# Kernel tuning notes

Hardware: AMD Instinct MI355X
Metric: run time of the kernel (lower is better)

Reference implementation:

```python
import jax, jax.numpy as jnp
import numpy as np

EPS = 1e-5

def setup_inputs() -> dict:
    key = jax.random.key(0)
    k1, k2 = jax.random.split(key)
    N, D, O = 32768, 4096, 256
    x = jax.random.normal(k1, (N, D), dtype=jnp.float32)
    gamma = jnp.ones((D,), dtype=jnp.float32)
    beta = jnp.zeros((D,), dtype=jnp.float32)
    W = jax.random.normal(k2, (O, D), dtype=jnp.float32) * (1.0 / np.sqrt(D))
    b = jnp.zeros((O,), dtype=jnp.float32)
    return {"x": x, "gamma": gamma, "beta": beta, "W": W, "b": b}


def reference(x, gamma, beta, W, b):
    # BatchNorm1d in training mode: per-feature batch mean and biased variance
    mean = jnp.mean(x, axis=0)                      # [D]
    var = jnp.mean(jnp.square(x - mean), axis=0)    # [D], biased (divide by N)
    xhat = (x - mean) * jax.lax.rsqrt(var + EPS)
    h = jax.nn.relu(xhat * gamma + beta)            # [N, D]
    # Linear projection
    return h @ W.T + b                               # [N, O]
```

## Files before the change

kernel.cpp:

```cpp
#include <hip/hip_runtime.h>
#include <hip/hip_bf16.h>

#define NROWS 32768
#define DDIM  4096
#define ODIM  256
#define EPSV  1e-5f

#define CHUNKS 128
#define RPC    256

#define BM 128
#define BK 64

typedef __attribute__((ext_vector_type(4))) float          f32x4;
typedef __attribute__((ext_vector_type(8))) __bf16         bf16x8;
typedef __attribute__((ext_vector_type(8))) unsigned short u16x8;
typedef __attribute__((ext_vector_type(4))) unsigned short u16x4;

static __device__ __forceinline__ unsigned short f2bf(float f) {
  return __builtin_bit_cast(unsigned short, __float2bfloat16(f));
}

__global__ __launch_bounds__(256) void k1_stats(const float* __restrict__ x,
                                                float* __restrict__ psum,
                                                float* __restrict__ psq) {
  const int col = blockIdx.x * 1024 + threadIdx.x * 4;
  const float* p = x + (size_t)blockIdx.y * RPC * DDIM + col;
  f32x4 s = {0.f, 0.f, 0.f, 0.f};
  f32x4 q = {0.f, 0.f, 0.f, 0.f};
#pragma unroll 8
  for (int r = 0; r < RPC; ++r) {
    f32x4 v = *(const f32x4*)p;
    p += DDIM;
    s += v;
    q += v * v;
  }
  *(f32x4*)(psum + (size_t)blockIdx.y * DDIM + col) = s;
  *(f32x4*)(psq  + (size_t)blockIdx.y * DDIM + col) = q;
}

__global__ __launch_bounds__(256) void k2_stats_finalize(
    const float* __restrict__ psum, const float* __restrict__ psq,
    const float* __restrict__ gamma, const float* __restrict__ beta,
    float* __restrict__ scale, float* __restrict__ shift) {
  __shared__ float ss[4][64];
  __shared__ float sq[4][64];
  const int lane = threadIdx.x & 63;
  const int g    = threadIdx.x >> 6;
  const int d    = blockIdx.x * 64 + lane;
  float s = 0.f, qq = 0.f;
  for (int c = g * 32; c < (g + 1) * 32; ++c) {
    s  += psum[(size_t)c * DDIM + d];
    qq += psq [(size_t)c * DDIM + d];
  }
  ss[g][lane] = s;
  sq[g][lane] = qq;
  __syncthreads();
  if (g == 0) {
    s  = ss[0][lane] + ss[1][lane] + ss[2][lane] + ss[3][lane];
    qq = sq[0][lane] + sq[1][lane] + sq[2][lane] + sq[3][lane];
    const float inv = 1.0f / (float)NROWS;
    const float mean = s * inv;
    const float var  = fmaxf(qq * inv - mean * mean, 0.f);
    const float a = gamma[d] * rsqrtf(var + EPSV);
    scale[d] = a;
    shift[d] = beta[d] - mean * a;
  }
}

__global__ __launch_bounds__(256) void k2_wconv(const float* __restrict__ Wf,
                                                unsigned short* __restrict__ Wb) {
  const size_t i = ((size_t)blockIdx.x * 256 + threadIdx.x) * 4;
  f32x4 v = *(const f32x4*)(Wf + i);
  u16x4 o;
  o[0] = f2bf(v[0]); o[1] = f2bf(v[1]); o[2] = f2bf(v[2]); o[3] = f2bf(v[3]);
  *(u16x4*)(Wb + i) = o;
}

__global__ __launch_bounds__(512, 2) void k3_bn_gemm(
    const float* __restrict__ x,
    const unsigned short* __restrict__ Wb,
    const float* __restrict__ scale,
    const float* __restrict__ shift,
    const float* __restrict__ bias,
    float* __restrict__ out) {
  __shared__ unsigned short As[BM * BK];
  __shared__ unsigned short Bs[ODIM * BK];

  const int tid = threadIdx.x;
  const int l   = tid & 63;
  const int w   = tid >> 6;
  const int wr  = w >> 2;
  const int wc  = w & 3;
  const size_t bm0 = (size_t)blockIdx.x * BM;

  const int rA = tid >> 3;
  const int uA = tid & 7;
  const float* xp0 = x + (bm0 + rA) * (size_t)DDIM + uA * 8;
  const float* xp1 = xp0 + (size_t)64 * DDIM;
  unsigned short* aw0 = &As[rA * 64 + ((uA ^ (rA & 7)) << 3)];
  unsigned short* aw1 = aw0 + 64 * 64;
  const float* sp = scale + uA * 8;
  const float* cp = shift + uA * 8;

  const unsigned short* bsrc[4];
  unsigned short* bdst[4];
#pragma unroll
  for (int q = 0; q < 4; ++q) {
    const int p  = w * 256 + q * 64 + l;
    const int o  = p >> 3;
    const int up = p & 7;
    bsrc[q] = Wb + (size_t)o * DDIM + ((up ^ (o & 7)) << 3);
    bdst[q] = &Bs[(w * 256 + q * 64) * 8];
  }

  int offA[4], offB[4];
#pragma unroll
  for (int i = 0; i < 4; ++i) {
    const int row = wr * 64 + i * 16 + (l & 15);
    offA[i] = row * 64 + (((l >> 4) ^ (row & 7)) << 3);
  }
#pragma unroll
  for (int j = 0; j < 4; ++j) {
    const int row = wc * 64 + j * 16 + (l & 15);
    offB[j] = row * 64 + (((l >> 4) ^ (row & 7)) << 3);
  }

  const f32x4 zero = {0.f, 0.f, 0.f, 0.f};
  f32x4 acc[4][4];
#pragma unroll
  for (int i = 0; i < 4; ++i)
#pragma unroll
    for (int j = 0; j < 4; ++j) acc[i][j] = zero;

  for (int kt = 0; kt < DDIM / BK; ++kt) {
#pragma unroll
    for (int q = 0; q < 4; ++q) {
      __builtin_amdgcn_global_load_lds(
          (__attribute__((address_space(1))) void*)bsrc[q],
          (__attribute__((address_space(3))) void*)bdst[q], 16, 0, 0);
      bsrc[q] += BK;
    }
    f32x4 sa0 = *(const f32x4*)sp;
    f32x4 sa1 = *(const f32x4*)(sp + 4);
    f32x4 sc0 = *(const f32x4*)cp;
    f32x4 sc1 = *(const f32x4*)(cp + 4);
    f32x4 v00 = *(const f32x4*)xp0;
    f32x4 v01 = *(const f32x4*)(xp0 + 4);
    f32x4 v10 = *(const f32x4*)xp1;
    f32x4 v11 = *(const f32x4*)(xp1 + 4);
    sp += BK; cp += BK; xp0 += BK; xp1 += BK;
    u16x8 pk0, pk1;
#pragma unroll
    for (int e = 0; e < 4; ++e) {
      pk0[e]     = f2bf(fmaxf(v00[e] * sa0[e] + sc0[e], 0.f));
      pk0[e + 4] = f2bf(fmaxf(v01[e] * sa1[e] + sc1[e], 0.f));
      pk1[e]     = f2bf(fmaxf(v10[e] * sa0[e] + sc0[e], 0.f));
      pk1[e + 4] = f2bf(fmaxf(v11[e] * sa1[e] + sc1[e], 0.f));
    }
    *(u16x8*)aw0 = pk0;
    *(u16x8*)aw1 = pk1;

    __syncthreads();

#pragma unroll
    for (int kk = 0; kk < 2; ++kk) {
      const int kx = kk << 5;
      bf16x8 af[4], bf[4];
#pragma unroll
      for (int i = 0; i < 4; ++i)
        af[i] = __builtin_bit_cast(bf16x8, *(const u16x8*)&As[offA[i] ^ kx]);
#pragma unroll
      for (int j = 0; j < 4; ++j)
        bf[j] = __builtin_bit_cast(bf16x8, *(const u16x8*)&Bs[offB[j] ^ kx]);
#pragma unroll
      for (int i = 0; i < 4; ++i)
#pragma unroll
        for (int j = 0; j < 4; ++j)
          acc[i][j] = __builtin_amdgcn_mfma_f32_16x16x32_bf16(af[i], bf[j], acc[i][j], 0, 0, 0);
    }

    __syncthreads();
  }

  const int cl = l & 15;
  const int rg = l >> 4;
#pragma unroll
  for (int j = 0; j < 4; ++j) {
    const int oc = wc * 64 + j * 16 + cl;
    const float bv = bias[oc];
#pragma unroll
    for (int i = 0; i < 4; ++i) {
      const size_t r0 = bm0 + wr * 64 + i * 16 + rg * 4;
#pragma unroll
      for (int rr = 0; rr < 4; ++rr) {
        out[(r0 + rr) * ODIM + oc] = acc[i][j][rr] + bv;
      }
    }
  }
}

extern "C" void kernel_launch(void* const* d_in, const int* in_sizes, int n_in,
                              void* d_out, int out_size, void* d_ws, size_t ws_size,
                              hipStream_t stream) {
  const float* x     = (const float*)d_in[0];
  const float* gamma = (const float*)d_in[1];
  const float* beta  = (const float*)d_in[2];
  const float* W     = (const float*)d_in[3];
  const float* b     = (const float*)d_in[4];
  float* out = (float*)d_out;

  float* psum  = (float*)d_ws;
  float* psq   = psum + (size_t)CHUNKS * DDIM;
  float* scale = psum + 2 * (size_t)CHUNKS * DDIM;
  float* shift = scale + DDIM;
  unsigned short* Wb = (unsigned short*)(shift + DDIM);

  k1_stats<<<dim3(4, CHUNKS), 256, 0, stream>>>(x, psum, psq);
  k2_stats_finalize<<<DDIM / 64, 256, 0, stream>>>(psum, psq, gamma, beta, scale, shift);
  k2_wconv<<<(ODIM * DDIM) / 1024, 256, 0, stream>>>(W, Wb);
  k3_bn_gemm<<<NROWS / BM, 512, 0, stream>>>(x, Wb, scale, shift, b, out);
}
```

Before: 260.9 us.

## Double-buffer GEMM LDS tiles with register prefetch and widen stats grid

The fused BN+GEMM kernel now uses two LDS buffers for the A and B tiles. It issues the next tile's global loads of x and W before running the MFMAs on the current tile, then writes the normalized bf16 values into the other buffer, so only one barrier per k-step is needed. The launch bound drops to one block per CU because LDS use doubles, which trades occupancy for software overlap of memory and compute. The stats kernel also switches to 2-wide loads and twice as many blocks to spread the column-sum pass across more workgroups.

After: 285.9 us. 1.1x slower.

```diff
diff --git a/kernel.cpp b/kernel.cpp
--- a/kernel.cpp
+++ b/kernel.cpp
@@ -11,7 +11,9 @@
 
 #define BM 128
 #define BK 64
-
+#define NKT (DDIM / BK)
+
+typedef __attribute__((ext_vector_type(2))) float          f32x2;
 typedef __attribute__((ext_vector_type(4))) float          f32x4;
 typedef __attribute__((ext_vector_type(8))) __bf16         bf16x8;
 typedef __attribute__((ext_vector_type(8))) unsigned short u16x8;
@@ -24,19 +26,19 @@
 __global__ __launch_bounds__(256) void k1_stats(const float* __restrict__ x,
                                                 float* __restrict__ psum,
                                                 float* __restrict__ psq) {
-  const int col = blockIdx.x * 1024 + threadIdx.x * 4;
+  const int col = blockIdx.x * 512 + threadIdx.x * 2;
   const float* p = x + (size_t)blockIdx.y * RPC * DDIM + col;
-  f32x4 s = {0.f, 0.f, 0.f, 0.f};
-  f32x4 q = {0.f, 0.f, 0.f, 0.f};
+  f32x2 s = {0.f, 0.f};
+  f32x2 q = {0.f, 0.f};
 #pragma unroll 8
   for (int r = 0; r < RPC; ++r) {
-    f32x4 v = *(const f32x4*)p;
+    f32x2 v = *(const f32x2*)p;
     p += DDIM;
     s += v;
     q += v * v;
   }
-  *(f32x4*)(psum + (size_t)blockIdx.y * DDIM + col) = s;
-  *(f32x4*)(psq  + (size_t)blockIdx.y * DDIM + col) = q;
+  *(f32x2*)(psum + (size_t)blockIdx.y * DDIM + col) = s;
+  *(f32x2*)(psq  + (size_t)blockIdx.y * DDIM + col) = q;
 }
 
 __global__ __launch_bounds__(256) void k2_stats_finalize(
@@ -77,15 +79,15 @@
   *(u16x4*)(Wb + i) = o;
 }
 
-__global__ __launch_bounds__(512, 2) void k3_bn_gemm(
+__global__ __launch_bounds__(512, 1) void k3_bn_gemm(
     const float* __restrict__ x,
     const unsigned short* __restrict__ Wb,
     const float* __restrict__ scale,
     const float* __restrict__ shift,
     const float* __restrict__ bias,
     float* __restrict__ out) {
-  __shared__ unsigned short As[BM * BK];
-  __shared__ unsigned short Bs[ODIM * BK];
+  __shared__ unsigned short As[2][BM * BK];
+  __shared__ unsigned short Bs[2][ODIM * BK];
 
   const int tid = threadIdx.x;
   const int l   = tid & 63;
@@ -98,20 +100,17 @@
   const int uA = tid & 7;
   const float* xp0 = x + (bm0 + rA) * (size_t)DDIM + uA * 8;
   const float* xp1 = xp0 + (size_t)64 * DDIM;
-  unsigned short* aw0 = &As[rA * 64 + ((uA ^ (rA & 7)) << 3)];
-  unsigned short* aw1 = aw0 + 64 * 64;
+  const int awo = rA * 64 + ((uA ^ (rA & 7)) << 3);
   const float* sp = scale + uA * 8;
   const float* cp = shift + uA * 8;
 
   const unsigned short* bsrc[4];
-  unsigned short* bdst[4];
 #pragma unroll
   for (int q = 0; q < 4; ++q) {
     const int p  = w * 256 + q * 64 + l;
     const int o  = p >> 3;
     const int up = p & 7;
     bsrc[q] = Wb + (size_t)o * DDIM + ((up ^ (o & 7)) << 3);
-    bdst[q] = &Bs[(w * 256 + q * 64) * 8];
   }
 
   int offA[4], offB[4];
@@ -133,23 +132,24 @@
 #pragma unroll
     for (int j = 0; j < 4; ++j) acc[i][j] = zero;
 
-  for (int kt = 0; kt < DDIM / BK; ++kt) {
-#pragma unroll
-    for (int q = 0; q < 4; ++q) {
-      __builtin_amdgcn_global_load_lds(
-          (__attribute__((address_space(1))) void*)bsrc[q],
-          (__attribute__((address_space(3))) void*)bdst[q], 16, 0, 0);
-      bsrc[q] += BK;
-    }
+  {
+    f32x4 v00 = *(const f32x4*)xp0;
+    f32x4 v01 = *(const f32x4*)(xp0 + 4);
+    f32x4 v10 = *(const f32x4*)xp1;
+    f32x4 v11 = *(const f32x4*)(xp1 + 4);
     f32x4 sa0 = *(const f32x4*)sp;
     f32x4 sa1 = *(const f32x4*)(sp + 4);
     f32x4 sc0 = *(const f32x4*)cp;
     f32x4 sc1 = *(const f32x4*)(cp + 4);
-    f32x4 v00 = *(const f32x4*)xp0;
-    f32x4 v01 = *(const f32x4*)(xp0 + 4);
-    f32x4 v10 = *(const f32x4*)xp1;
-    f32x4 v11 = *(const f32x4*)(xp1 + 4);
-    sp += BK; cp += BK; xp0 += BK; xp1 += BK;
+    xp0 += BK; xp1 += BK; sp += BK; cp += BK;
+#pragma unroll
+    for (int q = 0; q < 4; ++q) {
+      __builtin_amdgcn_global_load_lds(
+          (__attribute__((address_space(1))) void*)bsrc[q],
+          (__attribute__((address_space(3))) void*)(&Bs[0][(w * 256 + q * 64) * 8]),
+          16, 0, 0);
+      bsrc[q] += BK;
+    }
     u16x8 pk0, pk1;
 #pragma unroll
     for (int e = 0; e < 4; ++e) {
@@ -158,30 +158,75 @@
       pk1[e]     = f2bf(fmaxf(v10[e] * sa0[e] + sc0[e], 0.f));
       pk1[e + 4] = f2bf(fmaxf(v11[e] * sa1[e] + sc1[e], 0.f));
     }
-    *(u16x8*)aw0 = pk0;
-    *(u16x8*)aw1 = pk1;
-
+    *(u16x8*)&As[0][awo]        = pk0;
+    *(u16x8*)&As[0][awo + 4096] = pk1;
     __syncthreads();
-
-#pragma unroll
-    for (int kk = 0; kk < 2; ++kk) {
-      const int kx = kk << 5;
-      bf16x8 af[4], bf[4];
-#pragma unroll
-      for (int i = 0; i < 4; ++i)
-        af[i] = __builtin_bit_cast(bf16x8, *(const u16x8*)&As[offA[i] ^ kx]);
-#pragma unroll
-      for (int j = 0; j < 4; ++j)
-        bf[j] = __builtin_bit_cast(bf16x8, *(const u16x8*)&Bs[offB[j] ^ kx]);
-#pragma unroll
-      for (int i = 0; i < 4; ++i)
-#pragma unroll
-        for (int j = 0; j < 4; ++j)
-          acc[i][j] = __builtin_amdgcn_mfma_f32_16x16x32_bf16(af[i], bf[j], acc[i][j], 0, 0, 0);
-    }
-
-    __syncthreads();
-  }
+  }
+
+#define STEP(BUFI, PF)                                                         \
+  do {                                                                         \
+    f32x4 v00, v01, v10, v11, sa0, sa1, sc0, sc1;                              \
+    if (PF) {                                                                  \
+      v00 = *(const f32x4*)xp0;                                                \
+      v01 = *(const f32x4*)(xp0 + 4);                                          \
+      v10 = *(const f32x4*)xp1;                                                \
+      v11 = *(const f32x4*)(xp1 + 4);                                          \
+      sa0 = *(const f32x4*)sp;                                                 \
+      sa1 = *(const f32x4*)(sp + 4);                                           \
+      sc0 = *(const f32x4*)cp;                                                 \
+      sc1 = *(const f32x4*)(cp + 4);                                           \
+      xp0 += BK; xp1 += BK; sp += BK; cp += BK;                                \
+      _Pragma("unroll")                                                        \
+      for (int q = 0; q < 4; ++q) {                                            \
+        __builtin_amdgcn_global_load_lds(                                      \
+            (__attribute__((address_space(1))) void*)bsrc[q],                  \
+            (__attribute__((address_space(3))) void*)(                         \
+                &Bs[(BUFI) ^ 1][(w * 256 + q * 64) * 8]),                      \
+            16, 0, 0);                                                         \
+        bsrc[q] += BK;                                                         \
+      }                                                                        \
+    }                                                                          \
+    _Pragma("unroll")                                                          \
+    for (int kk = 0; kk < 2; ++kk) {                                           \
+      const int kx = kk << 5;                                                  \
+      bf16x8 af[4], bfr[4];                                                    \
+      _Pragma("unroll")                                                        \
+      for (int i = 0; i < 4; ++i)                                              \
+        af[i] = __builtin_bit_cast(bf16x8,                                     \
+                                   *(const u16x8*)&As[BUFI][offA[i] ^ kx]);    \
+      _Pragma("unroll")                                                        \
+      for (int j = 0; j < 4; ++j)                                              \
+        bfr[j] = __builtin_bit_cast(bf16x8,                                    \
+                                    *(const u16x8*)&Bs[BUFI][offB[j] ^ kx]);   \
+      _Pragma("unroll")                                                        \
+      for (int i = 0; i < 4; ++i)                                              \
+        _Pragma("unroll")                                                      \
+        for (int j = 0; j < 4; ++j)                                            \
+          acc[i][j] = __builtin_amdgcn_mfma_f32_16x16x32_bf16(                 \
+              af[i], bfr[j], acc[i][j], 0, 0, 0);                              \
+    }                                                                          \
+    if (PF) {                                                                  \
+      u16x8 pk0, pk1;                                                          \
+      _Pragma("unroll")                                                        \
+      for (int e = 0; e < 4; ++e) {                                            \
+        pk0[e]     = f2bf(fmaxf(v00[e] * sa0[e] + sc0[e], 0.f));               \
+        pk0[e + 4] = f2bf(fmaxf(v01[e] * sa1[e] + sc1[e], 0.f));               \
+        pk1[e]     = f2bf(fmaxf(v10[e] * sa0[e] + sc0[e], 0.f));               \
+        pk1[e + 4] = f2bf(fmaxf(v11[e] * sa1[e] + sc1[e], 0.f));               \
+      }                                                                        \
+      *(u16x8*)&As[(BUFI) ^ 1][awo]        = pk0;                              \
+      *(u16x8*)&As[(BUFI) ^ 1][awo + 4096] = pk1;                              \
+    }                                                                          \
+    __syncthreads();                                                           \
+  } while (0)
+
+  for (int kt = 0; kt < NKT - 2; kt += 2) {
+    STEP(0, true);
+    STEP(1, true);
+  }
+  STEP(0, true);
+  STEP(1, false);
+#undef STEP
 
   const int cl = l & 15;
   const int rg = l >> 4;
@@ -216,7 +261,7 @@
   float* shift = scale + DDIM;
   unsigned short* Wb = (unsigned short*)(shift + DDIM);
 
-  k1_stats<<<dim3(4, CHUNKS), 256, 0, stream>>>(x, psum, psq);
+  k1_stats<<<dim3(8, CHUNKS), 256, 0, stream>>>(x, psum, psq);
   k2_stats_finalize<<<DDIM / 64, 256, 0, stream>>>(psum, psq, gamma, beta, scale, shift);
   k2_wconv<<<(ODIM * DDIM) / 1024, 256, 0, stream>>>(W, Wb);
   k3_bn_gemm<<<NROWS / BM, 512, 0, stream>>>(x, Wb, scale, shift, b, out);
```

## Double-buffer LDS tiles and prefetch next K-tile during MFMA phase

Applied to the files above, without the earlier changes.

Restructures the fused BN+GEMM main loop into a two-stage software pipeline. The next tile's x loads (via inline-asm global loads) and W global-to-LDS copies are issued before the current tile's MFMAs, with explicit waitcnt and barriers so there is one barrier per step instead of two. Scale and shift are staged into shared memory once per block. The larger LDS footprint (double buffers plus 32 KB of scale/shift) forces occupancy down to one block per CU, and the handwritten waitcnt logic could be fragile.

Measured after the change: 239.2 us (median of 2 runs). 8.3% less time.

```diff
diff --git a/kernel.cpp b/kernel.cpp
--- a/kernel.cpp
+++ b/kernel.cpp
@@ -11,6 +11,7 @@
 
 #define BM 128
 #define BK 64
+#define NKT (DDIM / BK)
 
 typedef __attribute__((ext_vector_type(4))) float          f32x4;
 typedef __attribute__((ext_vector_type(8))) __bf16         bf16x8;
@@ -77,15 +78,17 @@
   *(u16x4*)(Wb + i) = o;
 }
 
-__global__ __launch_bounds__(512, 2) void k3_bn_gemm(
+__global__ __launch_bounds__(512, 1) void k3_bn_gemm(
     const float* __restrict__ x,
     const unsigned short* __restrict__ Wb,
     const float* __restrict__ scale,
     const float* __restrict__ shift,
     const float* __restrict__ bias,
     float* __restrict__ out) {
-  __shared__ unsigned short As[BM * BK];
-  __shared__ unsigned short Bs[ODIM * BK];
+  __shared__ unsigned short As[2][BM * BK];
+  __shared__ unsigned short Bs[2][ODIM * BK];
+  __shared__ float SF[DDIM];
+  __shared__ float SH[DDIM];
 
   const int tid = threadIdx.x;
   const int l   = tid & 63;
@@ -94,24 +97,25 @@
   const int wc  = w & 3;
   const size_t bm0 = (size_t)blockIdx.x * BM;
 
+  ((f32x4*)SF)[tid * 2]     = ((const f32x4*)scale)[tid * 2];
+  ((f32x4*)SF)[tid * 2 + 1] = ((const f32x4*)scale)[tid * 2 + 1];
+  ((f32x4*)SH)[tid * 2]     = ((const f32x4*)shift)[tid * 2];
+  ((f32x4*)SH)[tid * 2 + 1] = ((const f32x4*)shift)[tid * 2 + 1];
+
   const int rA = tid >> 3;
   const int uA = tid & 7;
   const float* xp0 = x + (bm0 + rA) * (size_t)DDIM + uA * 8;
   const float* xp1 = xp0 + (size_t)64 * DDIM;
-  unsigned short* aw0 = &As[rA * 64 + ((uA ^ (rA & 7)) << 3)];
-  unsigned short* aw1 = aw0 + 64 * 64;
-  const float* sp = scale + uA * 8;
-  const float* cp = shift + uA * 8;
+  const int awo = rA * 64 + ((uA ^ (rA & 7)) << 3);
+  int ktb = uA * 8;
 
   const unsigned short* bsrc[4];
-  unsigned short* bdst[4];
 #pragma unroll
   for (int q = 0; q < 4; ++q) {
     const int p  = w * 256 + q * 64 + l;
     const int o  = p >> 3;
     const int up = p & 7;
     bsrc[q] = Wb + (size_t)o * DDIM + ((up ^ (o & 7)) << 3);
-    bdst[q] = &Bs[(w * 256 + q * 64) * 8];
   }
 
   int offA[4], offB[4];
@@ -133,55 +137,110 @@
 #pragma unroll
     for (int j = 0; j < 4; ++j) acc[i][j] = zero;
 
-  for (int kt = 0; kt < DDIM / BK; ++kt) {
-#pragma unroll
-    for (int q = 0; q < 4; ++q) {
-      __builtin_amdgcn_global_load_lds(
-          (__attribute__((address_space(1))) void*)bsrc[q],
-          (__attribute__((address_space(3))) void*)bdst[q], 16, 0, 0);
-      bsrc[q] += BK;
-    }
-    f32x4 sa0 = *(const f32x4*)sp;
-    f32x4 sa1 = *(const f32x4*)(sp + 4);
-    f32x4 sc0 = *(const f32x4*)cp;
-    f32x4 sc1 = *(const f32x4*)(cp + 4);
-    f32x4 v00 = *(const f32x4*)xp0;
-    f32x4 v01 = *(const f32x4*)(xp0 + 4);
-    f32x4 v10 = *(const f32x4*)xp1;
-    f32x4 v11 = *(const f32x4*)(xp1 + 4);
-    sp += BK; cp += BK; xp0 += BK; xp1 += BK;
-    u16x8 pk0, pk1;
-#pragma unroll
-    for (int e = 0; e < 4; ++e) {
-      pk0[e]     = f2bf(fmaxf(v00[e] * sa0[e] + sc0[e], 0.f));
-      pk0[e + 4] = f2bf(fmaxf(v01[e] * sa1[e] + sc1[e], 0.f));
-      pk1[e]     = f2bf(fmaxf(v10[e] * sa0[e] + sc0[e], 0.f));
-      pk1[e + 4] = f2bf(fmaxf(v11[e] * sa1[e] + sc1[e], 0.f));
-    }
-    *(u16x8*)aw0 = pk0;
-    *(u16x8*)aw1 = pk1;
-
-    __syncthreads();
-
-#pragma unroll
-    for (int kk = 0; kk < 2; ++kk) {
-      const int kx = kk << 5;
-      bf16x8 af[4], bf[4];
-#pragma unroll
-      for (int i = 0; i < 4; ++i)
-        af[i] = __builtin_bit_cast(bf16x8, *(const u16x8*)&As[offA[i] ^ kx]);
-#pragma unroll
-      for (int j = 0; j < 4; ++j)
-        bf[j] = __builtin_bit_cast(bf16x8, *(const u16x8*)&Bs[offB[j] ^ kx]);
-#pragma unroll
-      for (int i = 0; i < 4; ++i)
-#pragma unroll
-        for (int j = 0; j < 4; ++j)
-          acc[i][j] = __builtin_amdgcn_mfma_f32_16x16x32_bf16(af[i], bf[j], acc[i][j], 0, 0, 0);
-    }
-
-    __syncthreads();
-  }
+#define ISSUE_A(V00, V01, V10, V11)                                            \
+  asm volatile("global_load_dwordx4 %0, %1, off" : "=v"(V00) : "v"(xp0));      \
+  asm volatile("global_load_dwordx4 %0, %1, off" : "=v"(V01) : "v"(xp0 + 4));  \
+  asm volatile("global_load_dwordx4 %0, %1, off" : "=v"(V10) : "v"(xp1));      \
+  asm volatile("global_load_dwordx4 %0, %1, off" : "=v"(V11) : "v"(xp1 + 4));  \
+  asm volatile("" ::: "memory");
+
+#define ISSUE_B(BUFI)                                                          \
+  _Pragma("unroll")                                                            \
+  for (int q = 0; q < 4; ++q) {                                                \
+    __builtin_amdgcn_global_load_lds(                                          \
+        (__attribute__((address_space(1))) void*)bsrc[q],                      \
+        (__attribute__((address_space(3))) void*)(                             \
+            &Bs[BUFI][(w * 256 + q * 64) * 8]),                                \
+        16, 0, 0);                                                             \
+    bsrc[q] += BK;                                                             \
+  }
+
+#define TRANSFORM_WRITE(BUFI, V00, V01, V10, V11)                              \
+  {                                                                            \
+    f32x4 sa0 = *(const f32x4*)&SF[ktb];                                       \
+    f32x4 sa1 = *(const f32x4*)&SF[ktb + 4];                                   \
+    f32x4 sc0 = *(const f32x4*)&SH[ktb];                                       \
+    f32x4 sc1 = *(const f32x4*)&SH[ktb + 4];                                   \
+    ktb += BK;                                                                 \
+    u16x8 pk0, pk1;                                                            \
+    _Pragma("unroll")                                                          \
+    for (int e = 0; e < 4; ++e) {                                              \
+      pk0[e]     = f2bf(fmaxf(V00[e] * sa0[e] + sc0[e], 0.f));                 \
+      pk0[e + 4] = f2bf(fmaxf(V01[e] * sa1[e] + sc1[e], 0.f));                 \
+      pk1[e]     = f2bf(fmaxf(V10[e] * sa0[e] + sc0[e], 0.f));                 \
+      pk1[e + 4] = f2bf(fmaxf(V11[e] * sa1[e] + sc1[e], 0.f));                 \
+    }                                                                          \
+    *(u16x8*)&As[BUFI][awo]        = pk0;                                      \
+    *(u16x8*)&As[BUFI][awo + 4096] = pk1;                                      \
+  }
+
+#define MFMA_PHASE(BUFI)                                                       \
+  _Pragma("unroll")                                                            \
+  for (int kk = 0; kk < 2; ++kk) {                                             \
+    const int kx = kk << 5;                                                    \
+    bf16x8 af[4], bfr[4];                                                      \
+    _Pragma("unroll")                                                          \
+    for (int i = 0; i < 4; ++i)                                                \
+      af[i] = __builtin_bit_cast(bf16x8,                                       \
+                                 *(const u16x8*)&As[BUFI][offA[i] ^ kx]);      \
+    _Pragma("unroll")                                                          \
+    for (int j = 0; j < 4; ++j)                                                \
+      bfr[j] = __builtin_bit_cast(bf16x8,                                      \
+                                  *(const u16x8*)&Bs[BUFI][offB[j] ^ kx]);     \
+    _Pragma("unroll")                                                          \
+    for (int i = 0; i < 4; ++i)                                                \
+      _Pragma("unroll")                                                        \
+      for (int j = 0; j < 4; ++j)                                              \
+        acc[i][j] = __builtin_amdgcn_mfma_f32_16x16x32_bf16(                   \
+            af[i], bfr[j], acc[i][j], 0, 0, 0);                                \
+  }
+
+  {
+    f32x4 v00, v01, v10, v11;
+    ISSUE_A(v00, v01, v10, v11);
+    ISSUE_B(0);
+    xp0 += BK; xp1 += BK;
+    asm volatile("s_waitcnt lgkmcnt(0)" ::: "memory");
+    __builtin_amdgcn_sched_barrier(0);
+    __builtin_amdgcn_s_barrier();
+    asm volatile("s_waitcnt vmcnt(4)" ::: "memory");
+    __builtin_amdgcn_sched_barrier(0);
+    TRANSFORM_WRITE(0, v00, v01, v10, v11);
+    asm volatile("s_waitcnt vmcnt(0) lgkmcnt(0)" ::: "memory");
+    __builtin_amdgcn_sched_barrier(0);
+    __builtin_amdgcn_s_barrier();
+  }
+
+#define STEP(CUR, PF)                                                          \
+  do {                                                                         \
+    f32x4 v00, v01, v10, v11;                                                  \
+    if (PF) {                                                                  \
+      ISSUE_A(v00, v01, v10, v11);                                             \
+      ISSUE_B((CUR) ^ 1);                                                      \
+      xp0 += BK; xp1 += BK;                                                    \
+    }                                                                          \
+    MFMA_PHASE(CUR);                                                           \
+    if (PF) {                                                                  \
+      asm volatile("s_waitcnt vmcnt(4)" ::: "memory");                         \
+      __builtin_amdgcn_sched_barrier(0);                                       \
+      TRANSFORM_WRITE((CUR) ^ 1, v00, v01, v10, v11);                          \
+    }                                                                          \
+    asm volatile("s_waitcnt vmcnt(0) lgkmcnt(0)" ::: "memory");                \
+    __builtin_amdgcn_sched_barrier(0);                                         \
+    __builtin_amdgcn_s_barrier();                                              \
+  } while (0)
+
+  for (int kt = 0; kt < NKT - 2; kt += 2) {
+    STEP(0, true);
+    STEP(1, true);
+  }
+  STEP(0, true);
+  STEP(1, false);
+#undef STEP
+#undef MFMA_PHASE
+#undef TRANSFORM_WRITE
+#undef ISSUE_B
+#undef ISSUE_A
 
   const int cl = l & 15;
   const int rg = l >> 4;
```
